# Performance work log

Hardware: AMD Instinct MI355X
Metric: run time of the kernel (lower is better)

Reference implementation:

```python
import jax, jax.numpy as jnp
import numpy as np
import math

N, E, S, V, H, R = 10000, 160000, 512, 128, 8, 32
HD = S // H
CUTOFF = 10.0


def bessel_basis(d):
    # d: [E] -> [E, R], Bessel RBF with cosine cutoff
    freqs = jnp.arange(1, R + 1, dtype=d.dtype) * np.pi / CUTOFF  # [R]
    d1 = d[:, None]
    b = jnp.sin(freqs * d1) / jnp.maximum(d1, 1e-8)
    cut = 0.5 * (jnp.cos(np.pi * d1 / CUTOFF) + 1.0) * (d1 < CUTOFF).astype(d.dtype)
    return b * cut


def segment_softmax(logits, seg, num_seg):
    # logits: [E, H], seg: [E] destination node ids
    m = jax.ops.segment_max(logits, seg, num_segments=num_seg)
    m = jnp.where(jnp.isfinite(m), m, 0.0)
    e = jnp.exp(logits - m[seg])
    s = jax.ops.segment_sum(e, seg, num_segments=num_seg)
    return e / (s[seg] + 1e-9)


def layernorm(x, g, b, eps=1e-5):
    mu = jnp.mean(x, axis=-1, keepdims=True)
    var = jnp.mean(jnp.square(x - mu), axis=-1, keepdims=True)
    return (x - mu) * jax.lax.rsqrt(var + eps) * g + b


def setup_inputs() -> dict:
    key = jax.random.key(0)
    ks = jax.random.split(key, 24)
    sc = lambda fan_in: 1.0 / math.sqrt(fan_in)
    inp = {
        "scalars": jax.random.normal(ks[0], (N, S), jnp.float32),
        "vectors": jax.random.normal(ks[1], (N, V, 3), jnp.float32),
        "edge_vec": jax.random.normal(ks[2], (E, 3), jnp.float32),
        "Wq_s": jax.random.normal(ks[3], (S, S), jnp.float32) * sc(S),
        "bq_s": jnp.zeros((S,), jnp.float32),
        "Wk_s": jax.random.normal(ks[4], (S, S), jnp.float32) * sc(S),
        "bk_s": jnp.zeros((S,), jnp.float32),
        "Wv_s": jax.random.normal(ks[5], (S, S), jnp.float32) * sc(S),
        "bv_s": jnp.zeros((S,), jnp.float32),
        "Wq_v": jax.random.normal(ks[6], (V, V), jnp.float32) * sc(V),
        "Wk_v": jax.random.normal(ks[7], (V, V), jnp.float32) * sc(V),
        "Wv_v": jax.random.normal(ks[8], (V, V), jnp.float32) * sc(V),
        "Wout_s": jax.random.normal(ks[9], (S, S), jnp.float32) * sc(S),
        "bout_s": jnp.zeros((S,), jnp.float32),
        "Wout_v": jax.random.normal(ks[10], (V, V), jnp.float32) * sc(V),
        "bout_v": jnp.zeros((V,), jnp.float32),
        "W_edge": jax.random.normal(ks[11], (R, H), jnp.float32) * sc(R),
        "b_edge": jnp.zeros((H,), jnp.float32),
        "ln_g": jnp.ones((S,), jnp.float32),
        "ln_b": jnp.zeros((S,), jnp.float32),
        "edge_index": jax.random.randint(ks[12], (2, E), 0, N, jnp.int64),
    }
    return inp


def reference(scalars, vectors, edge_vec, Wq_s, bq_s, Wk_s, bk_s, Wv_s, bv_s,
              Wq_v, Wk_v, Wv_v, Wout_s, bout_s, Wout_v, bout_v,
              W_edge, b_edge, ln_g, ln_b, edge_index):
    row, col = edge_index[0], edge_index[1]
    edge_dist = jnp.linalg.norm(edge_vec, axis=-1)  # [E]

    # scalar Q/K/V, split into heads
    q_s = (scalars @ Wq_s + bq_s).reshape(N, H, HD)
    k_s = (scalars @ Wk_s + bk_s).reshape(N, H, HD)
    v_s = (scalars @ Wv_s + bv_s).reshape(N, H, HD)

    # vector Q/K/V: channel-mixing linear over the num_vectors axis (equivariant in 3D)
    q_v = jnp.einsum('nvi,vw->nwi', vectors, Wq_v)
    k_v = jnp.einsum('nvi,vw->nwi', vectors, Wk_v)
    v_v = jnp.einsum('nvi,vw->nwi', vectors, Wv_v)

    # per-edge attention logits
    att_s = jnp.einsum('ehd,ehd->eh', q_s[row], k_s[col])          # [E,H]
    att_v = jnp.einsum('evi,evi->e', q_v[row], k_v[col]) / math.sqrt(3.0)
    edge_att = bessel_basis(edge_dist) @ W_edge + b_edge            # [E,H]
    logits = (att_s + att_v[:, None] + edge_att) / math.sqrt(HD)

    # softmax over incoming edges of each destination node (row)
    attn = segment_softmax(logits, row, N)                          # [E,H]

    # scalar messages (per-head)
    msg_s = attn[:, :, None] * v_s[col]                             # [E,H,HD]
    out_s = jax.ops.segment_sum(msg_s, row, num_segments=N).reshape(N, S)
    out_s = out_s @ Wout_s + bout_s

    # vector messages (head-averaged attention, scalar gate keeps equivariance)
    a_v = jnp.mean(attn, axis=-1)                                   # [E]
    msg_v = a_v[:, None, None] * v_v[col]                           # [E,V,3]
    out_v = jax.ops.segment_sum(msg_v, row, num_segments=N)         # [N,V,3]
    out_v = jnp.einsum('nvi,vw->nwi', out_v, Wout_v) + bout_v[None, :, None]

    scalars_out = layernorm(scalars + out_s, ln_g, ln_b)
    vectors_out = vectors + out_v
    return scalars_out, vectors_out
```

## Files before the change

kernel.cpp:

```cpp
#include <hip/hip_runtime.h>
#include <math.h>

#define N_NODES 10000
#define E_EDGES 160000
#define S_DIM 512
#define QKV3 (3*S_DIM)
#define V_DIM 128
#define VQKV3 (3*V_DIM)
#define H_HEADS 8
#define R_BASIS 32
#define HD_DIM 64
#define NV3 (V_DIM*3)
#define KV8P 896

typedef _Float16 f16;
typedef f16 f16x2 __attribute__((ext_vector_type(2)));
typedef f16 f16x8 __attribute__((ext_vector_type(8)));
typedef float f32x4 __attribute__((ext_vector_type(4)));
typedef float fl2 __attribute__((ext_vector_type(2)));

static __device__ __forceinline__ float h2f(unsigned short u) {
  f16 h; __builtin_memcpy(&h, &u, 2); return (float)h;
}
static __device__ __forceinline__ unsigned short f2h(float f) {
  f16 h = (f16)f; unsigned short u; __builtin_memcpy(&u, &h, 2); return u;
}
static __device__ __forceinline__ float wave_sum(float v) {
  #pragma unroll
  for (int o = 32; o > 0; o >>= 1) v += __shfl_xor(v, o, 64);
  return v;
}
static __device__ __forceinline__ float wave_max(float v) {
  #pragma unroll
  for (int o = 32; o > 0; o >>= 1) v = fmaxf(v, __shfl_xor(v, o, 64));
  return v;
}
static __device__ __forceinline__ float dot_i4(int4 a, int4 b, float s) {
  union U { int4 v; f16x2 h[4]; } ua, ub;
  ua.v = a; ub.v = b;
  #pragma unroll
  for (int j = 0; j < 4; ++j)
    s = __builtin_amdgcn_fdot2(ua.h[j], ub.h[j], s, false);
  return s;
}
static __device__ __forceinline__ void glds16(const unsigned short* g, unsigned short* l) {
  __builtin_amdgcn_global_load_lds(
      (const __attribute__((address_space(1))) unsigned int*)g,
      (__attribute__((address_space(3))) unsigned int*)l, 16, 0, 0);
}

__global__ __launch_bounds__(256) void prep_kernel(
    const float* __restrict__ scalars, unsigned short* __restrict__ Af16,
    const int* __restrict__ ei, int* __restrict__ counts,
    const float* __restrict__ bq, const float* __restrict__ bk,
    const float* __restrict__ bv, float* __restrict__ bias_cat)
{
  int b = blockIdx.x, t = threadIdx.x;
  if (b < 5000) {
    int i = b * 256 + t;
    float4 v = reinterpret_cast<const float4*>(scalars)[i];
    ushort4 o;
    o.x = f2h(v.x); o.y = f2h(v.y); o.z = f2h(v.z); o.w = f2h(v.w);
    reinterpret_cast<ushort4*>(Af16)[i] = o;
  } else if (b < 5625) {
    int e = (b - 5000) * 256 + t;
    if (e < E_EDGES) atomicAdd(&counts[ei[e]], 1);
  } else {
    int c = (b - 5625) * 256 + t;
    if (c < QKV3)
      bias_cat[c] = (c < 512) ? bq[c] : (c < 1024) ? bk[c - 512] : bv[c - 1024];
  }
}

__global__ __launch_bounds__(256) void transpose4_kernel(
    const float* __restrict__ W0, const float* __restrict__ W1,
    const float* __restrict__ W2, const float* __restrict__ W3,
    unsigned short* __restrict__ Dcat, unsigned short* __restrict__ Do, int D)
{
  __shared__ float t[32][33];
  int z = blockIdx.z;
  const float* W = (z == 0) ? W0 : (z == 1) ? W1 : (z == 2) ? W2 : W3;
  unsigned short* dst = (z < 3) ? Dcat + (size_t)z * D * D : Do;
  int n0 = blockIdx.x * 32, k0 = blockIdx.y * 32;
  int x = threadIdx.x, y = threadIdx.y;
  #pragma unroll
  for (int j = 0; j < 32; j += 8)
    t[y + j][x] = W[(size_t)(k0 + y + j) * D + n0 + x];
  __syncthreads();
  #pragma unroll
  for (int j = 0; j < 32; j += 8)
    dst[(size_t)(n0 + y + j) * D + k0 + x] = f2h(t[x][y + j]);
}

__global__ __launch_bounds__(128) void vec_transpose_kernel(
    const float* __restrict__ vecs, unsigned short* __restrict__ VT)
{
  __shared__ float l[NV3];
  int n = blockIdx.x, t = threadIdx.x;
  #pragma unroll
  for (int j = 0; j < 3; ++j) l[t + j * 128] = vecs[(size_t)n * NV3 + t + j * 128];
  __syncthreads();
  #pragma unroll
  for (int i = 0; i < 3; ++i)
    VT[((size_t)n * 3 + i) * V_DIM + t] = f2h(l[t * 3 + i]);
}

__global__ __launch_bounds__(256) void gemm_f16_kernel(
    const unsigned short* __restrict__ A, const unsigned short* __restrict__ Bt,
    const float* __restrict__ bias, float* __restrict__ Cf,
    unsigned short* __restrict__ Ch, int M, int K, int Nn)
{
  __shared__ unsigned short lds[2][2][128 * 32];
  int tid = threadIdx.x;
  int wid = tid >> 6, lane = tid & 63;
  int wr = wid >> 1, wc = wid & 1;
  int row0 = blockIdx.y * 128, col0 = blockIdx.x * 128;

  int r0 = tid >> 2, s0 = tid & 3;
  int r1 = r0 + 64;
  int sw0 = (r0 >> 1) & 3;
  int aoff = (s0 ^ sw0) * 8;
  int gra0 = row0 + r0; if (gra0 >= M) gra0 = M - 1;
  int gra1 = row0 + r1; if (gra1 >= M) gra1 = M - 1;
  const unsigned short* ag0 = A + (size_t)gra0 * K + aoff;
  const unsigned short* ag1 = A + (size_t)gra1 * K + aoff;
  const unsigned short* bg0 = Bt + (size_t)(col0 + r0) * K + aoff;
  const unsigned short* bg1 = Bt + (size_t)(col0 + r1) * K + aoff;

  f32x4 acc[4][4];
  #pragma unroll
  for (int m = 0; m < 4; ++m)
    #pragma unroll
    for (int n = 0; n < 4; ++n) acc[m][n] = (f32x4){0.f, 0.f, 0.f, 0.f};

  int lr = lane & 15, lq = lane >> 4;
  int slot = (lq ^ ((lr >> 1) & 3)) * 8;
  int aro[4], bro[4];
  #pragma unroll
  for (int m = 0; m < 4; ++m) aro[m] = (wr * 64 + m * 16 + lr) * 32 + slot;
  #pragma unroll
  for (int n = 0; n < 4; ++n) bro[n] = (wc * 64 + n * 16 + lr) * 32 + slot;

  int nk = K >> 5;
  glds16(ag0, &lds[0][0][tid * 8]);
  glds16(ag1, &lds[0][0][(tid + 256) * 8]);
  glds16(bg0, &lds[0][1][tid * 8]);
  glds16(bg1, &lds[0][1][(tid + 256) * 8]);
  __syncthreads();

  for (int t = 0; t < nk; ++t) {
    int cur = t & 1;
    if (t + 1 < nk) {
      int ko = (t + 1) << 5;
      glds16(ag0 + ko, &lds[cur ^ 1][0][tid * 8]);
      glds16(ag1 + ko, &lds[cur ^ 1][0][(tid + 256) * 8]);
      glds16(bg0 + ko, &lds[cur ^ 1][1][tid * 8]);
      glds16(bg1 + ko, &lds[cur ^ 1][1][(tid + 256) * 8]);
    }
    const unsigned short* Ab = lds[cur][0];
    const unsigned short* Bb = lds[cur][1];
    f16x8 af[4], bf[4];
    #pragma unroll
    for (int m = 0; m < 4; ++m) af[m] = *reinterpret_cast<const f16x8*>(Ab + aro[m]);
    #pragma unroll
    for (int n = 0; n < 4; ++n) bf[n] = *reinterpret_cast<const f16x8*>(Bb + bro[n]);
    #pragma unroll
    for (int m = 0; m < 4; ++m)
      #pragma unroll
      for (int n = 0; n < 4; ++n)
        acc[m][n] = __builtin_amdgcn_mfma_f32_16x16x32_f16(af[m], bf[n], acc[m][n], 0, 0, 0);
    __syncthreads();
  }

  float bcol[4];
  #pragma unroll
  for (int n = 0; n < 4; ++n)
    bcol[n] = bias ? bias[col0 + wc * 64 + n * 16 + lr] : 0.f;
  int rl = tid >> 3, cc = (tid & 7) * 16;

  if (Cf) {
    float* cst = reinterpret_cast<float*>(&lds[0][0][0]);
    #pragma unroll
    for (int m = 0; m < 4; ++m) {
      __syncthreads();
      #pragma unroll
      for (int n = 0; n < 4; ++n)
        #pragma unroll
        for (int j = 0; j < 4; ++j)
          cst[(wr * 16 + lq * 4 + j) * 128 + wc * 64 + n * 16 + lr] = acc[m][n][j] + bcol[n];
      __syncthreads();
      int row = row0 + (rl >> 4) * 64 + m * 16 + (rl & 15);
      if (row < M) {
        float4* dst = reinterpret_cast<float4*>(Cf + (size_t)row * Nn + col0 + cc);
        const float4* src = reinterpret_cast<const float4*>(cst + rl * 128 + cc);
        dst[0] = src[0]; dst[1] = src[1]; dst[2] = src[2]; dst[3] = src[3];
      }
    }
  } else {
    unsigned short* csth = &lds[0][0][0];
    #pragma unroll
    for (int m = 0; m < 4; ++m) {
      __syncthreads();
      #pragma unroll
      for (int n = 0; n < 4; ++n)
        #pragma unroll
        for (int j = 0; j < 4; ++j)
          csth[(wr * 16 + lq * 4 + j) * 128 + wc * 64 + n * 16 + lr] = f2h(acc[m][n][j] + bcol[n]);
      __syncthreads();
      int row = row0 + (rl >> 4) * 64 + m * 16 + (rl & 15);
      if (row < M) {
        int4* dst = reinterpret_cast<int4*>(Ch + (size_t)row * Nn + col0 + cc);
        const int4* src = reinterpret_cast<const int4*>(csth + rl * 128 + cc);
        dst[0] = src[0]; dst[1] = src[1];
      }
    }
  }
}

__global__ __launch_bounds__(256) void pack_v8_kernel(
    const unsigned short* __restrict__ qkv_s, const unsigned short* __restrict__ qkv_v,
    unsigned char* __restrict__ v8)
{
  int t = threadIdx.x;
  int j = t & 127;
  if (j >= 112) return;
  int n = blockIdx.x * 2 + (t >> 7);
  int c = j * 8;
  const unsigned short* src;
  if (c < 512) {
    src = qkv_s + (size_t)n * QKV3 + 1024 + c;
  } else {
    int cc = c - 512, i = cc >> 7, w = cc & 127;
    src = qkv_v + ((size_t)n * 3 + i) * VQKV3 + 256 + w;
  }
  int4 sv = *reinterpret_cast<const int4*>(src);
  union { int4 v; unsigned short u[8]; } us; us.v = sv;
  float f[8];
  #pragma unroll
  for (int q = 0; q < 8; ++q) f[q] = h2f(us.u[q]);
  unsigned int d0 = (unsigned)__builtin_amdgcn_cvt_pk_fp8_f32(f[0], f[1], 0, false);
  d0 = (unsigned)__builtin_amdgcn_cvt_pk_fp8_f32(f[2], f[3], (int)d0, true);
  unsigned int d1 = (unsigned)__builtin_amdgcn_cvt_pk_fp8_f32(f[4], f[5], 0, false);
  d1 = (unsigned)__builtin_amdgcn_cvt_pk_fp8_f32(f[6], f[7], (int)d1, true);
  uint2 o; o.x = d0; o.y = d1;
  *reinterpret_cast<uint2*>(v8 + (size_t)n * KV8P + c) = o;
}

__global__ __launch_bounds__(1024) void scan_kernel(const int* __restrict__ counts,
                                                    int* __restrict__ offs) {
  __shared__ int wsum[16];
  __shared__ int carry_s;
  int tid = threadIdx.x;
  int lane = tid & 63, w = tid >> 6;
  if (tid == 0) carry_s = 0;
  __syncthreads();
  for (int base = 0; base < N_NODES; base += 1024) {
    int i = base + tid;
    int v = (i < N_NODES) ? counts[i] : 0;
    int x = v;
    #pragma unroll
    for (int o = 1; o < 64; o <<= 1) {
      int t = __shfl_up(x, o, 64);
      if (lane >= o) x += t;
    }
    if (lane == 63) wsum[w] = x;
    __syncthreads();
    if (w == 0 && lane < 16) {
      int t = wsum[lane];
      #pragma unroll
      for (int o = 1; o < 16; o <<= 1) {
        int u = __shfl_up(t, o, 64);
        if (lane >= o) t += u;
      }
      wsum[lane] = t;
    }
    __syncthreads();
    int incl = x + ((w > 0) ? wsum[w - 1] : 0);
    int c = carry_s;
    __syncthreads();
    if (i < N_NODES) offs[i] = c + incl - v;
    if (tid == 1023) carry_s = c + incl;
    __syncthreads();
  }
  if (tid == 0) offs[N_NODES] = carry_s;
}

__global__ void scatter_kernel(const int* __restrict__ ei, const int* __restrict__ offs,
                               int* __restrict__ cursor, int* __restrict__ eord) {
  int e = blockIdx.x * 256 + threadIdx.x;
  if (e < E_EDGES) {
    int r = ei[e];
    int p = offs[r] + atomicAdd(&cursor[r], 1);
    eord[p] = e;
  }
}

__global__ __launch_bounds__(256, 4) void edge_logits_kernel(
    const unsigned short* __restrict__ qkv_s, const unsigned short* __restrict__ qkv_v,
    const float* __restrict__ edge_vec, const int* __restrict__ ei,
    const int* __restrict__ eord,
    const float* __restrict__ W_edge, const float* __restrict__ b_edge,
    float* __restrict__ logits, int* __restrict__ cols)
{
  __shared__ float Wl[R_BASIS * H_HEADS];
  Wl[threadIdx.x] = W_edge[threadIdx.x];
  __syncthreads();

  int lane = threadIdx.x & 63;
  int wv = threadIdx.x >> 6;
  int g = lane >> 3, h = lane & 7;
  int pos = blockIdx.x * 32 + wv * 8 + g;
  int e = eord[pos];
  int row = ei[e], col = ei[E_EDGES + e];

  const unsigned short* qp = qkv_s + (size_t)row * QKV3 + h * HD_DIM;
  const unsigned short* kp = qkv_s + (size_t)col * QKV3 + 512 + h * HD_DIM;
  int4 qa[8], ka[8];
  #pragma unroll
  for (int r = 0; r < 8; ++r) qa[r] = *reinterpret_cast<const int4*>(qp + r * 8);
  #pragma unroll
  for (int r = 0; r < 8; ++r) ka[r] = *reinterpret_cast<const int4*>(kp + r * 8);

  int4 qv[6], kv[6];
  #pragma unroll
  for (int r = 0; r < 6; ++r) {
    int f = h * 48 + r * 8;
    int i = f >> 7, w = f & 127;
    qv[r] = *reinterpret_cast<const int4*>(qkv_v + ((size_t)row * 3 + i) * VQKV3 + w);
    kv[r] = *reinterpret_cast<const int4*>(qkv_v + ((size_t)col * 3 + i) * VQKV3 + 128 + w);
  }

  float ex = edge_vec[(size_t)e * 3 + 0];
  float ey = edge_vec[(size_t)e * 3 + 1];
  float ez = edge_vec[(size_t)e * 3 + 2];

  float qk = 0.f;
  #pragma unroll
  for (int r = 0; r < 8; ++r) qk = dot_i4(qa[r], ka[r], qk);

  float pv = 0.f;
  #pragma unroll
  for (int r = 0; r < 6; ++r) pv = dot_i4(qv[r], kv[r], pv);
  pv += __shfl_xor(pv, 1, 64);
  pv += __shfl_xor(pv, 2, 64);
  pv += __shfl_xor(pv, 4, 64);
  pv *= 0.57735026918962576f;

  float d = sqrtf(ex * ex + ey * ey + ez * ez);
  float th = d * 0.31415926535897932f;
  float s1 = __sinf(th), c1 = __cosf(th);
  float s2 = 2.f * s1 * c1,         c2 = fmaf(c1, c1, -s1 * s1);
  float s3 = fmaf(s2, c1, c2 * s1), c3 = fmaf(c2, c1, -s2 * s1);
  float s4 = 2.f * s2 * c2,         c4 = fmaf(c2, c2, -s2 * s2);
  float sr[4] = {s1, s2, s3, s4};
  float cr[4] = {c1, c2, c3, c4};
  float acc = 0.f;
  #pragma unroll
  for (int t = 0; t < 8; ++t) {
    #pragma unroll
    for (int j = 0; j < 4; ++j) {
      acc = fmaf(sr[j], Wl[(t * 4 + j) * H_HEADS + h], acc);
      float sn = fmaf(sr[j], c4, cr[j] * s4);
      cr[j] = fmaf(cr[j], c4, -sr[j] * s4);
      sr[j] = sn;
    }
  }
  float cut = (d < 10.f) ? 0.5f * (c1 + 1.f) : 0.f;
  float eah = fmaf(acc, cut / fmaxf(d, 1e-8f), b_edge[h]);

  logits[(size_t)pos * H_HEADS + h] = (qk + pv + eah) * 0.125f;
  if (h == 0) cols[pos] = col;
}

#define MAXDEG 512
__global__ __launch_bounds__(256) void agg_kernel(
    const float* __restrict__ logits, const int* __restrict__ cols,
    const unsigned char* __restrict__ v8, const int* __restrict__ offs,
    unsigned short* __restrict__ out_s, unsigned short* __restrict__ out_v)
{
  __shared__ float attn_lds[MAXDEG * H_HEADS];
  __shared__ float av_lds[MAXDEG];
  __shared__ int col_lds[MAXDEG];
  __shared__ float m_sh[H_HEADS], inv_sh[H_HEADS];

  int n = blockIdx.x;
  int beg = offs[n];
  int deg = offs[n + 1] - beg;
  int tid = threadIdx.x;
  bool fits = (deg <= MAXDEG);

  if (tid < 64) {
    int lane = tid;
    float lm[H_HEADS];
    #pragma unroll
    for (int h = 0; h < H_HEADS; ++h) lm[h] = -INFINITY;
    for (int i = lane; i < deg; i += 64) {
      const float4* lp = reinterpret_cast<const float4*>(logits + (size_t)(beg + i) * 8);
      float4 a = lp[0], b = lp[1];
      if (fits) col_lds[i] = cols[beg + i];
      lm[0] = fmaxf(lm[0], a.x); lm[1] = fmaxf(lm[1], a.y);
      lm[2] = fmaxf(lm[2], a.z); lm[3] = fmaxf(lm[3], a.w);
      lm[4] = fmaxf(lm[4], b.x); lm[5] = fmaxf(lm[5], b.y);
      lm[6] = fmaxf(lm[6], b.z); lm[7] = fmaxf(lm[7], b.w);
    }
    #pragma unroll
    for (int h = 0; h < H_HEADS; ++h) lm[h] = wave_max(lm[h]);

    float ls[H_HEADS];
    #pragma unroll
    for (int h = 0; h < H_HEADS; ++h) ls[h] = 0.f;
    for (int i = lane; i < deg; i += 64) {
      const float4* lp = reinterpret_cast<const float4*>(logits + (size_t)(beg + i) * 8);
      float4 a = lp[0], b = lp[1];
      float w[8];
      w[0] = expf(a.x - lm[0]); w[1] = expf(a.y - lm[1]);
      w[2] = expf(a.z - lm[2]); w[3] = expf(a.w - lm[3]);
      w[4] = expf(b.x - lm[4]); w[5] = expf(b.y - lm[5]);
      w[6] = expf(b.z - lm[6]); w[7] = expf(b.w - lm[7]);
      #pragma unroll
      for (int h = 0; h < H_HEADS; ++h) {
        ls[h] += w[h];
        if (fits) attn_lds[i * 8 + h] = w[h];
      }
    }
    #pragma unroll
    for (int h = 0; h < H_HEADS; ++h) ls[h] = wave_sum(ls[h]);

    float inv[H_HEADS];
    #pragma unroll
    for (int h = 0; h < H_HEADS; ++h) inv[h] = 1.f / (ls[h] + 1e-9f);
    if (lane == 0) {
      #pragma unroll
      for (int h = 0; h < H_HEADS; ++h) { m_sh[h] = lm[h]; inv_sh[h] = inv[h]; }
    }
    if (fits) {
      for (int i = lane; i < deg; i += 64) {
        float a = 0.f;
        #pragma unroll
        for (int h = 0; h < H_HEADS; ++h) a += attn_lds[i * 8 + h] * inv[h];
        av_lds[i] = 0.125f * a;
      }
    }
  }
  __syncthreads();

  int lane = tid & 63, wv = tid >> 6;
  int h = lane >> 3;
  float ih = inv_sh[h], mh = m_sh[h];
  float accs[8] = {0,0,0,0,0,0,0,0};
  float accv[8] = {0,0,0,0,0,0,0,0};

  auto body = [&](int i) {
    int colv;
    float wgt, av;
    if (fits) {
      colv = col_lds[i];
      wgt = attn_lds[i * 8 + h] * ih;
      av = av_lds[i];
    } else {
      colv = cols[beg + i];
      const float* lp = logits + (size_t)(beg + i) * 8;
      wgt = expf(lp[h] - mh) * ih;
      float a = 0.f;
      #pragma unroll
      for (int hh = 0; hh < H_HEADS; ++hh)
        a += expf(lp[hh] - m_sh[hh]) * inv_sh[hh];
      av = 0.125f * a;
    }
    uint2 vs = *reinterpret_cast<const uint2*>(v8 + (size_t)colv * KV8P + lane * 8);
    fl2 b0 = __builtin_amdgcn_cvt_pk_f32_fp8(vs.x, false);
    fl2 b1 = __builtin_amdgcn_cvt_pk_f32_fp8(vs.x, true);
    fl2 b2 = __builtin_amdgcn_cvt_pk_f32_fp8(vs.y, false);
    fl2 b3 = __builtin_amdgcn_cvt_pk_f32_fp8(vs.y, true);
    accs[0] = fmaf(wgt, b0.x, accs[0]); accs[1] = fmaf(wgt, b0.y, accs[1]);
    accs[2] = fmaf(wgt, b1.x, accs[2]); accs[3] = fmaf(wgt, b1.y, accs[3]);
    accs[4] = fmaf(wgt, b2.x, accs[4]); accs[5] = fmaf(wgt, b2.y, accs[5]);
    accs[6] = fmaf(wgt, b3.x, accs[6]); accs[7] = fmaf(wgt, b3.y, accs[7]);
    if (lane < 48) {
      uint2 vv = *reinterpret_cast<const uint2*>(v8 + (size_t)colv * KV8P + 512 + lane * 8);
      fl2 c0 = __builtin_amdgcn_cvt_pk_f32_fp8(vv.x, false);
      fl2 c1 = __builtin_amdgcn_cvt_pk_f32_fp8(vv.x, true);
      fl2 c2 = __builtin_amdgcn_cvt_pk_f32_fp8(vv.y, false);
      fl2 c3 = __builtin_amdgcn_cvt_pk_f32_fp8(vv.y, true);
      accv[0] = fmaf(av, c0.x, accv[0]); accv[1] = fmaf(av, c0.y, accv[1]);
      accv[2] = fmaf(av, c1.x, accv[2]); accv[3] = fmaf(av, c1.y, accv[3]);
      accv[4] = fmaf(av, c2.x, accv[4]); accv[5] = fmaf(av, c2.y, accv[5]);
      accv[6] = fmaf(av, c3.x, accv[6]); accv[7] = fmaf(av, c3.y, accv[7]);
    }
  };

  int i = wv;
  for (; i + 4 < deg; i += 8) { body(i); body(i + 4); }
  if (i < deg) body(i);
  __syncthreads();

  float* red_s = attn_lds;
  float* red_v = attn_lds + 2048;
  #pragma unroll
  for (int j = 0; j < 8; j += 4)
    *reinterpret_cast<float4*>(&red_s[wv * 512 + lane * 8 + j]) =
      make_float4(accs[j], accs[j+1], accs[j+2], accs[j+3]);
  if (lane < 48) {
    #pragma unroll
    for (int j = 0; j < 8; j += 4)
      *reinterpret_cast<float4*>(&red_v[wv * 384 + lane * 8 + j]) =
        make_float4(accv[j], accv[j+1], accv[j+2], accv[j+3]);
  }
  __syncthreads();

  {
    int d0 = 2 * tid;
    float s0 = red_s[d0] + red_s[512 + d0] + red_s[1024 + d0] + red_s[1536 + d0];
    float s1 = red_s[d0+1] + red_s[512 + d0+1] + red_s[1024 + d0+1] + red_s[1536 + d0+1];
    ushort2 o; o.x = f2h(s0); o.y = f2h(s1);
    *reinterpret_cast<ushort2*>(out_s + (size_t)n * S_DIM + d0) = o;
  }
  if (tid < 192) {
    int d0 = 2 * tid;
    float s0 = red_v[d0] + red_v[384 + d0] + red_v[768 + d0] + red_v[1152 + d0];
    float s1 = red_v[d0+1] + red_v[384 + d0+1] + red_v[768 + d0+1] + red_v[1152 + d0+1];
    ushort2 o; o.x = f2h(s0); o.y = f2h(s1);
    *reinterpret_cast<ushort2*>(out_v + (size_t)n * NV3 + d0) = o;
  }
}

__global__ __launch_bounds__(128) void vec_epilogue_kernel(
    const float* __restrict__ tmp, const float* __restrict__ bout_v,
    const float* __restrict__ vectors, float* __restrict__ out)
{
  __shared__ float l[NV3];
  int n = blockIdx.x, t = threadIdx.x;
  #pragma unroll
  for (int i = 0; i < 3; ++i)
    l[i * 128 + t] = tmp[((size_t)n * 3 + i) * V_DIM + t];
  __syncthreads();
  #pragma unroll
  for (int c = 0; c < 3; ++c) {
    int j = t + c * 128;
    int w = j / 3, i = j - 3 * w;
    out[(size_t)n * NV3 + j] = l[i * 128 + w] + bout_v[w] + vectors[(size_t)n * NV3 + j];
  }
}

__global__ __launch_bounds__(256) void ln_kernel(
    const float* __restrict__ x0, const float* __restrict__ dx,
    const float* __restrict__ g, const float* __restrict__ b,
    float* __restrict__ out)
{
  int r = blockIdx.x * 4 + (threadIdx.x >> 6);
  int lane = threadIdx.x & 63;
  if (r >= N_NODES) return;
  float x[8];
  float s = 0.f;
  #pragma unroll
  for (int j = 0; j < 8; ++j) {
    int d = lane + j * 64;
    x[j] = x0[(size_t)r * S_DIM + d] + dx[(size_t)r * S_DIM + d];
    s += x[j];
  }
  s = wave_sum(s);
  float mu = s * (1.f / 512.f);
  float vs = 0.f;
  #pragma unroll
  for (int j = 0; j < 8; ++j) { float t = x[j] - mu; vs += t * t; }
  vs = wave_sum(vs);
  float inv = rsqrtf(vs * (1.f / 512.f) + 1e-5f);
  #pragma unroll
  for (int j = 0; j < 8; ++j) {
    int d = lane + j * 64;
    out[(size_t)r * S_DIM + d] = (x[j] - mu) * inv * g[d] + b[d];
  }
}

extern "C" void kernel_launch(void* const* d_in, const int* in_sizes, int n_in,
                              void* d_out, int out_size, void* d_ws, size_t ws_size,
                              hipStream_t stream)
{
  (void)in_sizes; (void)n_in; (void)out_size; (void)ws_size;
  const float* scalars  = (const float*)d_in[0];
  const float* vectors  = (const float*)d_in[1];
  const float* edge_vec = (const float*)d_in[2];
  const float* Wq_s = (const float*)d_in[3];
  const float* bq_s = (const float*)d_in[4];
  const float* Wk_s = (const float*)d_in[5];
  const float* bk_s = (const float*)d_in[6];
  const float* Wv_s = (const float*)d_in[7];
  const float* bv_s = (const float*)d_in[8];
  const float* Wq_v = (const float*)d_in[9];
  const float* Wk_v = (const float*)d_in[10];
  const float* Wv_v = (const float*)d_in[11];
  const float* Wout_s = (const float*)d_in[12];
  const float* bout_s = (const float*)d_in[13];
  const float* Wout_v = (const float*)d_in[14];
  const float* bout_v = (const float*)d_in[15];
  const float* W_edge = (const float*)d_in[16];
  const float* b_edge = (const float*)d_in[17];
  const float* ln_g = (const float*)d_in[18];
  const float* ln_b = (const float*)d_in[19];
  const int* ei = (const int*)d_in[20];

  float* out = (float*)d_out;
  const size_t NS  = (size_t)N_NODES * S_DIM;
  const size_t NVs = (size_t)N_NODES * NV3;
  const size_t EH  = (size_t)E_EDGES * H_HEADS;
  const size_t WSZ = (size_t)S_DIM * S_DIM;
  const size_t WVZ = (size_t)V_DIM * V_DIM;
  const int MV = N_NODES * 3;

  char* base = (char*)d_ws;
  auto carve = [&](size_t bytes) -> char* {
    char* p = base;
    base += (bytes + 255) & ~(size_t)255;
    return p;
  };
  unsigned short* Af16 = (unsigned short*)carve(NS * 2);
  unsigned short* VT0  = (unsigned short*)carve(NVs * 2);
  float* tmpv = (float*)Af16;
  unsigned short* qkv_s = (unsigned short*)carve((size_t)N_NODES * QKV3 * 2);
  unsigned short* qkv_v = (unsigned short*)carve((size_t)MV * VQKV3 * 2);
  unsigned short* outs_pre = (unsigned short*)carve(NS * 2);
  unsigned short* outv_pre = (unsigned short*)carve(NVs * 2);
  float* dx       = (float*)carve(NS * 4);
  unsigned char* v8 = (unsigned char*)dx;
  float* logitsS  = (float*)carve(EH * 4);
  int*   colsS    = (int*)carve(E_EDGES * 4);
  unsigned short* WqkvT  = (unsigned short*)carve(3 * WSZ * 2);
  unsigned short* WoT    = (unsigned short*)carve(WSZ * 2);
  unsigned short* WqkvvT = (unsigned short*)carve(3 * WVZ * 2);
  unsigned short* WovT   = (unsigned short*)carve(WVZ * 2);
  float* bias_cat = (float*)carve(QKV3 * 4);
  int* counts = (int*)carve(N_NODES * 4);
  int* offs   = (int*)carve((N_NODES + 1) * 4);
  int* cursor = (int*)carve(N_NODES * 4);
  int* eord   = (int*)carve(E_EDGES * 4);

  hipMemsetAsync(counts, 0, N_NODES * sizeof(int), stream);
  hipMemsetAsync(cursor, 0, N_NODES * sizeof(int), stream);

  prep_kernel<<<5631, 256, 0, stream>>>(scalars, Af16, ei, counts,
                                        bq_s, bk_s, bv_s, bias_cat);
  dim3 tBlk(32, 8);
  transpose4_kernel<<<dim3(16, 16, 4), tBlk, 0, stream>>>(Wq_s, Wk_s, Wv_s, Wout_s, WqkvT, WoT, S_DIM);
  transpose4_kernel<<<dim3(4, 4, 4), tBlk, 0, stream>>>(Wq_v, Wk_v, Wv_v, Wout_v, WqkvvT, WovT, V_DIM);
  vec_transpose_kernel<<<N_NODES, 128, 0, stream>>>(vectors, VT0);

  gemm_f16_kernel<<<dim3(QKV3 / 128, (N_NODES + 127) / 128), 256, 0, stream>>>(
      Af16, WqkvT, bias_cat, nullptr, qkv_s, N_NODES, S_DIM, QKV3);
  gemm_f16_kernel<<<dim3(VQKV3 / 128, (MV + 127) / 128), 256, 0, stream>>>(
      VT0, WqkvvT, nullptr, nullptr, qkv_v, MV, V_DIM, VQKV3);

  pack_v8_kernel<<<N_NODES / 2, 256, 0, stream>>>(qkv_s, qkv_v, v8);

  scan_kernel<<<1, 1024, 0, stream>>>(counts, offs);
  scatter_kernel<<<(E_EDGES + 255) / 256, 256, 0, stream>>>(ei, offs, cursor, eord);

  edge_logits_kernel<<<E_EDGES / 32, 256, 0, stream>>>(qkv_s, qkv_v, edge_vec,
                                                       ei, eord, W_edge, b_edge,
                                                       logitsS, colsS);

  agg_kernel<<<N_NODES, 256, 0, stream>>>(logitsS, colsS, v8, offs,
                                          outs_pre, outv_pre);

  gemm_f16_kernel<<<dim3(S_DIM / 128, (N_NODES + 127) / 128), 256, 0, stream>>>(
      outs_pre, WoT, bout_s, dx, nullptr, N_NODES, S_DIM, S_DIM);
  gemm_f16_kernel<<<dim3(1, (MV + 127) / 128), 256, 0, stream>>>(
      outv_pre, WovT, nullptr, tmpv, nullptr, MV, V_DIM, V_DIM);
  vec_epilogue_kernel<<<N_NODES, 128, 0, stream>>>(tmpv, bout_v, vectors, out + NS);
  ln_kernel<<<2500, 256, 0, stream>>>(scalars, dx, ln_g, ln_b, out);
}
```

Before: 276.7 us.

## Quantize Q/K/V to per-node int8 and use sdot4 for edge logits

Replaces the fp8 V packing with a per-node, per-tensor symmetric int8 quantization of Q, K and V, storing scales separately. The edge logits kernel now gathers int8 Q/K (half the bytes of fp16) and computes dot products with integer sdot4, applying scales afterwards. The aggregation kernel dequantizes int8 V by folding the per-node scale into the weight. This cuts gather bandwidth in the edge stage but adds quantization error to the attention logits and a heavier packing kernel.

```diff
diff --git a/kernel.cpp b/kernel.cpp
--- a/kernel.cpp
+++ b/kernel.cpp
@@ -17,7 +17,6 @@
 typedef f16 f16x2 __attribute__((ext_vector_type(2)));
 typedef f16 f16x8 __attribute__((ext_vector_type(8)));
 typedef float f32x4 __attribute__((ext_vector_type(4)));
-typedef float fl2 __attribute__((ext_vector_type(2)));
 
 static __device__ __forceinline__ float h2f(unsigned short u) {
   f16 h; __builtin_memcpy(&h, &u, 2); return (float)h;
@@ -35,14 +34,29 @@
   for (int o = 32; o > 0; o >>= 1) v = fmaxf(v, __shfl_xor(v, o, 64));
   return v;
 }
-static __device__ __forceinline__ float dot_i4(int4 a, int4 b, float s) {
-  union U { int4 v; f16x2 h[4]; } ua, ub;
-  ua.v = a; ub.v = b;
+
+#if defined(__has_builtin)
+#if __has_builtin(__builtin_amdgcn_sdot4)
+#define SDOT4(a, b, c) __builtin_amdgcn_sdot4((int)(a), (int)(b), (c), false)
+#endif
+#endif
+#ifndef SDOT4
+static __device__ __forceinline__ int sdot4_sw(unsigned int a, unsigned int b, int c) {
   #pragma unroll
   for (int j = 0; j < 4; ++j)
-    s = __builtin_amdgcn_fdot2(ua.h[j], ub.h[j], s, false);
-  return s;
-}
+    c += (int)(char)((a >> (8 * j)) & 0xff) * (int)(char)((b >> (8 * j)) & 0xff);
+  return c;
+}
+#define SDOT4(a, b, c) sdot4_sw((a), (b), (c))
+#endif
+
+static __device__ __forceinline__ void fma_i8x4(unsigned int w, float wt, float* acc) {
+  acc[0] = fmaf(wt, (float)(int)(char)(w & 0xff), acc[0]);
+  acc[1] = fmaf(wt, (float)(int)(char)((w >> 8) & 0xff), acc[1]);
+  acc[2] = fmaf(wt, (float)(int)(char)((w >> 16) & 0xff), acc[2]);
+  acc[3] = fmaf(wt, (float)(int)(char)((w >> 24) & 0xff), acc[3]);
+}
+
 static __device__ __forceinline__ void glds16(const unsigned short* g, unsigned short* l) {
   __builtin_amdgcn_global_load_lds(
       (const __attribute__((address_space(1))) unsigned int*)g,
@@ -217,33 +231,73 @@
   }
 }
 
-__global__ __launch_bounds__(256) void pack_v8_kernel(
+__global__ __launch_bounds__(256) void pack_i8_kernel(
     const unsigned short* __restrict__ qkv_s, const unsigned short* __restrict__ qkv_v,
-    unsigned char* __restrict__ v8)
-{
-  int t = threadIdx.x;
-  int j = t & 127;
-  if (j >= 112) return;
-  int n = blockIdx.x * 2 + (t >> 7);
-  int c = j * 8;
-  const unsigned short* src;
-  if (c < 512) {
-    src = qkv_s + (size_t)n * QKV3 + 1024 + c;
-  } else {
-    int cc = c - 512, i = cc >> 7, w = cc & 127;
-    src = qkv_v + ((size_t)n * 3 + i) * VQKV3 + 256 + w;
-  }
-  int4 sv = *reinterpret_cast<const int4*>(src);
-  union { int4 v; unsigned short u[8]; } us; us.v = sv;
-  float f[8];
-  #pragma unroll
-  for (int q = 0; q < 8; ++q) f[q] = h2f(us.u[q]);
-  unsigned int d0 = (unsigned)__builtin_amdgcn_cvt_pk_fp8_f32(f[0], f[1], 0, false);
-  d0 = (unsigned)__builtin_amdgcn_cvt_pk_fp8_f32(f[2], f[3], (int)d0, true);
-  unsigned int d1 = (unsigned)__builtin_amdgcn_cvt_pk_fp8_f32(f[4], f[5], 0, false);
-  d1 = (unsigned)__builtin_amdgcn_cvt_pk_fp8_f32(f[6], f[7], (int)d1, true);
-  uint2 o; o.x = d0; o.y = d1;
-  *reinterpret_cast<uint2*>(v8 + (size_t)n * KV8P + c) = o;
+    char* __restrict__ q8, char* __restrict__ k8, char* __restrict__ v8,
+    float* __restrict__ scales)
+{
+  __shared__ float am[336];
+  __shared__ float inv_sh[3];
+  int n = blockIdx.x, t = threadIdx.x;
+  float va[2][8];
+
+  auto loadChunk = [&](int chunk, float* v) {
+    int r = chunk / 112, j = chunk - r * 112;
+    int c = j * 8;
+    const unsigned short* src;
+    if (c < 512) {
+      src = qkv_s + (size_t)n * QKV3 + r * 512 + c;
+    } else {
+      int cc = c - 512, i = cc >> 7, w = cc & 127;
+      src = qkv_v + ((size_t)n * 3 + i) * VQKV3 + r * 128 + w;
+    }
+    int4 sv = *reinterpret_cast<const int4*>(src);
+    union { int4 x; unsigned short u[8]; } us; us.x = sv;
+    float m = 0.f;
+    #pragma unroll
+    for (int q = 0; q < 8; ++q) { v[q] = h2f(us.u[q]); m = fmaxf(m, fabsf(v[q])); }
+    am[chunk] = m;
+  };
+
+  loadChunk(t, va[0]);
+  if (t < 80) loadChunk(256 + t, va[1]);
+  __syncthreads();
+
+  int lane = t & 63, wid = t >> 6;
+  if (wid < 3) {
+    int basec = wid * 112;
+    float m = am[basec + lane];
+    if (lane < 48) m = fmaxf(m, am[basec + 64 + lane]);
+    m = wave_max(m);
+    if (lane == 0) {
+      m = fmaxf(m, 1e-8f);
+      scales[3 * n + wid] = m * (1.f / 127.f);
+      inv_sh[wid] = 127.f / m;
+    }
+  }
+  __syncthreads();
+
+  auto quantStore = [&](int chunk, const float* v) {
+    int r = chunk / 112, j = chunk - r * 112;
+    float inv = inv_sh[r];
+    unsigned int b0 = 0, b1 = 0;
+    #pragma unroll
+    for (int q = 0; q < 4; ++q) {
+      int x = __float2int_rn(v[q] * inv);
+      b0 |= ((unsigned)(x & 0xff)) << (8 * q);
+    }
+    #pragma unroll
+    for (int q = 0; q < 4; ++q) {
+      int x = __float2int_rn(v[4 + q] * inv);
+      b1 |= ((unsigned)(x & 0xff)) << (8 * q);
+    }
+    char* dst = (r == 0 ? q8 : r == 1 ? k8 : v8) + (size_t)n * KV8P + j * 8;
+    uint2 o; o.x = b0; o.y = b1;
+    *reinterpret_cast<uint2*>(dst) = o;
+  };
+
+  quantStore(t, va[0]);
+  if (t < 80) quantStore(256 + t, va[1]);
 }
 
 __global__ __launch_bounds__(1024) void scan_kernel(const int* __restrict__ counts,
@@ -296,7 +350,8 @@
 }
 
 __global__ __launch_bounds__(256, 4) void edge_logits_kernel(
-    const unsigned short* __restrict__ qkv_s, const unsigned short* __restrict__ qkv_v,
+    const char* __restrict__ q8, const char* __restrict__ k8,
+    const float* __restrict__ scales,
     const float* __restrict__ edge_vec, const int* __restrict__ ei,
     const int* __restrict__ eord,
     const float* __restrict__ W_edge, const float* __restrict__ b_edge,
@@ -313,38 +368,49 @@
   int e = eord[pos];
   int row = ei[e], col = ei[E_EDGES + e];
 
-  const unsigned short* qp = qkv_s + (size_t)row * QKV3 + h * HD_DIM;
-  const unsigned short* kp = qkv_s + (size_t)col * QKV3 + 512 + h * HD_DIM;
-  int4 qa[8], ka[8];
-  #pragma unroll
-  for (int r = 0; r < 8; ++r) qa[r] = *reinterpret_cast<const int4*>(qp + r * 8);
-  #pragma unroll
-  for (int r = 0; r < 8; ++r) ka[r] = *reinterpret_cast<const int4*>(kp + r * 8);
-
-  int4 qv[6], kv[6];
-  #pragma unroll
-  for (int r = 0; r < 6; ++r) {
-    int f = h * 48 + r * 8;
-    int i = f >> 7, w = f & 127;
-    qv[r] = *reinterpret_cast<const int4*>(qkv_v + ((size_t)row * 3 + i) * VQKV3 + w);
-    kv[r] = *reinterpret_cast<const int4*>(qkv_v + ((size_t)col * 3 + i) * VQKV3 + 128 + w);
-  }
-
+  const char* qp = q8 + (size_t)row * KV8P + h * HD_DIM;
+  const char* kp = k8 + (size_t)col * KV8P + h * HD_DIM;
+  uint4 qa[4], ka[4];
+  #pragma unroll
+  for (int r = 0; r < 4; ++r) qa[r] = *reinterpret_cast<const uint4*>(qp + r * 16);
+  #pragma unroll
+  for (int r = 0; r < 4; ++r) ka[r] = *reinterpret_cast<const uint4*>(kp + r * 16);
+
+  const char* qvp = q8 + (size_t)row * KV8P + 512 + h * 48;
+  const char* kvp = k8 + (size_t)col * KV8P + 512 + h * 48;
+  uint4 qv[3], kv[3];
+  #pragma unroll
+  for (int r = 0; r < 3; ++r) qv[r] = *reinterpret_cast<const uint4*>(qvp + r * 16);
+  #pragma unroll
+  for (int r = 0; r < 3; ++r) kv[r] = *reinterpret_cast<const uint4*>(kvp + r * 16);
+
+  float sq = scales[3 * row + 0];
+  float sk = scales[3 * col + 1];
   float ex = edge_vec[(size_t)e * 3 + 0];
   float ey = edge_vec[(size_t)e * 3 + 1];
   float ez = edge_vec[(size_t)e * 3 + 2];
 
-  float qk = 0.f;
-  #pragma unroll
-  for (int r = 0; r < 8; ++r) qk = dot_i4(qa[r], ka[r], qk);
-
-  float pv = 0.f;
-  #pragma unroll
-  for (int r = 0; r < 6; ++r) pv = dot_i4(qv[r], kv[r], pv);
-  pv += __shfl_xor(pv, 1, 64);
-  pv += __shfl_xor(pv, 2, 64);
-  pv += __shfl_xor(pv, 4, 64);
-  pv *= 0.57735026918962576f;
+  int dsum = 0;
+  #pragma unroll
+  for (int r = 0; r < 4; ++r) {
+    dsum = SDOT4(qa[r].x, ka[r].x, dsum);
+    dsum = SDOT4(qa[r].y, ka[r].y, dsum);
+    dsum = SDOT4(qa[r].z, ka[r].z, dsum);
+    dsum = SDOT4(qa[r].w, ka[r].w, dsum);
+  }
+  int dvec = 0;
+  #pragma unroll
+  for (int r = 0; r < 3; ++r) {
+    dvec = SDOT4(qv[r].x, kv[r].x, dvec);
+    dvec = SDOT4(qv[r].y, kv[r].y, dvec);
+    dvec = SDOT4(qv[r].z, kv[r].z, dvec);
+    dvec = SDOT4(qv[r].w, kv[r].w, dvec);
+  }
+  dvec += __shfl_xor(dvec, 1, 64);
+  dvec += __shfl_xor(dvec, 2, 64);
+  dvec += __shfl_xor(dvec, 4, 64);
+
+  float att = sq * sk * ((float)dsum + 0.57735026918962576f * (float)dvec);
 
   float d = sqrtf(ex * ex + ey * ey + ez * ez);
   float th = d * 0.31415926535897932f;
@@ -368,14 +434,15 @@
   float cut = (d < 10.f) ? 0.5f * (c1 + 1.f) : 0.f;
   float eah = fmaf(acc, cut / fmaxf(d, 1e-8f), b_edge[h]);
 
-  logits[(size_t)pos * H_HEADS + h] = (qk + pv + eah) * 0.125f;
+  logits[(size_t)pos * H_HEADS + h] = (att + eah) * 0.125f;
   if (h == 0) cols[pos] = col;
 }
 
 #define MAXDEG 512
 __global__ __launch_bounds__(256) void agg_kernel(
     const float* __restrict__ logits, const int* __restrict__ cols,
-    const unsigned char* __restrict__ v8, const int* __restrict__ offs,
+    const char* __restrict__ v8, const float* __restrict__ scales,
+    const int* __restrict__ offs,
     unsigned short* __restrict__ out_s, unsigned short* __restrict__ out_v)
 {
   __shared__ float attn_lds[MAXDEG * H_HEADS];
@@ -467,25 +534,15 @@
         a += expf(lp[hh] - m_sh[hh]) * inv_sh[hh];
       av = 0.125f * a;
     }
+    float svc = scales[3 * colv + 2];
+    wgt *= svc; av *= svc;
     uint2 vs = *reinterpret_cast<const uint2*>(v8 + (size_t)colv * KV8P + lane * 8);
-    fl2 b0 = __builtin_amdgcn_cvt_pk_f32_fp8(vs.x, false);
-    fl2 b1 = __builtin_amdgcn_cvt_pk_f32_fp8(vs.x, true);
-    fl2 b2 = __builtin_amdgcn_cvt_pk_f32_fp8(vs.y, false);
-    fl2 b3 = __builtin_amdgcn_cvt_pk_f32_fp8(vs.y, true);
-    accs[0] = fmaf(wgt, b0.x, accs[0]); accs[1] = fmaf(wgt, b0.y, accs[1]);
-    accs[2] = fmaf(wgt, b1.x, accs[2]); accs[3] = fmaf(wgt, b1.y, accs[3]);
-    accs[4] = fmaf(wgt, b2.x, accs[4]); accs[5] = fmaf(wgt, b2.y, accs[5]);
-    accs[6] = fmaf(wgt, b3.x, accs[6]); accs[7] = fmaf(wgt, b3.y, accs[7]);
+    fma_i8x4(vs.x, wgt, accs);
+    fma_i8x4(vs.y, wgt, accs + 4);
     if (lane < 48) {
-      uint2 vv = *reinterpret_cast<const uint2*>(v8 + (size_t)colv * KV8P + 512 + lane * 8);
-      fl2 c0 = __builtin_amdgcn_cvt_pk_f32_fp8(vv.x, false);
-      fl2 c1 = __builtin_amdgcn_cvt_pk_f32_fp8(vv.x, true);
-      fl2 c2 = __builtin_amdgcn_cvt_pk_f32_fp8(vv.y, false);
-      fl2 c3 = __builtin_amdgcn_cvt_pk_f32_fp8(vv.y, true);
-      accv[0] = fmaf(av, c0.x, accv[0]); accv[1] = fmaf(av, c0.y, accv[1]);
-      accv[2] = fmaf(av, c1.x, accv[2]); accv[3] = fmaf(av, c1.y, accv[3]);
-      accv[4] = fmaf(av, c2.x, accv[4]); accv[5] = fmaf(av, c2.y, accv[5]);
-      accv[6] = fmaf(av, c3.x, accv[6]); accv[7] = fmaf(av, c3.y, accv[7]);
+      uint2 vvl = *reinterpret_cast<const uint2*>(v8 + (size_t)colv * KV8P + 512 + lane * 8);
+      fma_i8x4(vvl.x, av, accv);
+      fma_i8x4(vvl.y, av, accv + 4);
     }
   };
 
@@ -616,12 +673,14 @@
   unsigned short* Af16 = (unsigned short*)carve(NS * 2);
   unsigned short* VT0  = (unsigned short*)carve(NVs * 2);
   float* tmpv = (float*)Af16;
+  char* v8 = (char*)Af16;
   unsigned short* qkv_s = (unsigned short*)carve((size_t)N_NODES * QKV3 * 2);
   unsigned short* qkv_v = (unsigned short*)carve((size_t)MV * VQKV3 * 2);
   unsigned short* outs_pre = (unsigned short*)carve(NS * 2);
   unsigned short* outv_pre = (unsigned short*)carve(NVs * 2);
   float* dx       = (float*)carve(NS * 4);
-  unsigned char* v8 = (unsigned char*)dx;
+  char* q8 = (char*)dx;
+  char* k8 = q8 + (size_t)N_NODES * KV8P;
   float* logitsS  = (float*)carve(EH * 4);
   int*   colsS    = (int*)carve(E_EDGES * 4);
   unsigned short* WqkvT  = (unsigned short*)carve(3 * WSZ * 2);
@@ -629,6 +688,7 @@
   unsigned short* WqkvvT = (unsigned short*)carve(3 * WVZ * 2);
   unsigned short* WovT   = (unsigned short*)carve(WVZ * 2);
   float* bias_cat = (float*)carve(QKV3 * 4);
+  float* scales   = (float*)carve(3 * N_NODES * 4);
   int* counts = (int*)carve(N_NODES * 4);
   int* offs   = (int*)carve((N_NODES + 1) * 4);
   int* cursor = (int*)carve(N_NODES * 4);
@@ -649,16 +709,16 @@
   gemm_f16_kernel<<<dim3(VQKV3 / 128, (MV + 127) / 128), 256, 0, stream>>>(
       VT0, WqkvvT, nullptr, nullptr, qkv_v, MV, V_DIM, VQKV3);
 
-  pack_v8_kernel<<<N_NODES / 2, 256, 0, stream>>>(qkv_s, qkv_v, v8);
+  pack_i8_kernel<<<N_NODES, 256, 0, stream>>>(qkv_s, qkv_v, q8, k8, v8, scales);
 
   scan_kernel<<<1, 1024, 0, stream>>>(counts, offs);
   scatter_kernel<<<(E_EDGES + 255) / 256, 256, 0, stream>>>(ei, offs, cursor, eord);
 
-  edge_logits_kernel<<<E_EDGES / 32, 256, 0, stream>>>(qkv_s, qkv_v, edge_vec,
+  edge_logits_kernel<<<E_EDGES / 32, 256, 0, stream>>>(q8, k8, scales, edge_vec,
                                                        ei, eord, W_edge, b_edge,
                                                        logitsS, colsS);
 
-  agg_kernel<<<N_NODES, 256, 0, stream>>>(logitsS, colsS, v8, offs,
+  agg_kernel<<<N_NODES, 256, 0, stream>>>(logitsS, colsS, v8, scales, offs,
                                           outs_pre, outv_pre);
 
   gemm_f16_kernel<<<dim3(S_DIM / 128, (N_NODES + 127) / 128), 256, 0, stream>>>(
```

Result: faster. 247.3 us (-10.6%).
